# Kernel tuning notes

Measured on AMD Instinct MI355X. Metric: run time of the kernel, lower is better.

## Reference

```python
import jax, jax.numpy as jnp
import numpy as np

N_NODES = 100000


def _gcn_conv(x, row, col, W, b, n):
    # PyG GCNConv: h = W x; out_i = sum_{j->i} norm_ij * h_j + b, with self-loops
    # and symmetric normalization norm_ij = deg_i^-1/2 * deg_j^-1/2.
    h = x @ W  # [N, out]
    loop = jnp.arange(n, dtype=row.dtype)
    r = jnp.concatenate([row, loop])
    c = jnp.concatenate([col, loop])
    deg = jax.ops.segment_sum(jnp.ones_like(c, dtype=h.dtype), c, num_segments=n)
    dinv = jnp.where(deg > 0, jax.lax.rsqrt(deg), 0.0)
    norm = dinv[r] * dinv[c]  # [E+N]
    msg = h[r] * norm[:, None]  # gather + per-edge scale
    out = jax.ops.segment_sum(msg, c, num_segments=n)  # scatter-add to dst
    return out + b


def setup_inputs() -> dict:
    key = jax.random.key(0)
    ks = jax.random.split(key, 8)
    N, E = N_NODES, 1600000
    d_in, comm_dim, hid, out = 120, 8, 128, 64
    x = jax.random.normal(ks[0], (N, d_in), dtype=jnp.float32)
    edge_index = jax.random.randint(ks[1], (2, E), 0, N, dtype=jnp.int64)
    comm_ids = jax.random.randint(ks[2], (N,), 0, 64, dtype=jnp.int64)
    comm_emb = jax.random.normal(ks[3], (64, comm_dim), dtype=jnp.float32)
    s1 = 1.0 / np.sqrt(d_in + comm_dim)
    s2 = 1.0 / np.sqrt(hid)
    W1 = jax.random.normal(ks[4], (d_in + comm_dim, hid), dtype=jnp.float32) * s1
    b1 = jnp.zeros((hid,), dtype=jnp.float32)
    W2 = jax.random.normal(ks[5], (hid, out), dtype=jnp.float32) * s2
    b2 = jnp.zeros((out,), dtype=jnp.float32)
    return {"x": x, "edge_index": edge_index, "comm_ids": comm_ids,
            "comm_emb": comm_emb, "W1": W1, "b1": b1, "W2": W2, "b2": b2}


def reference(x, edge_index, comm_ids, comm_emb, W1, b1, W2, b2):
    n = x.shape[0]
    row, col = edge_index[0], edge_index[1]
    c = comm_emb[comm_ids]                      # [N, comm_dim] embedding lookup
    h = jnp.concatenate([x, c], axis=-1)        # [N, in+comm_dim]
    h = jax.nn.relu(_gcn_conv(h, row, col, W1, b1, n))
    # dropout p=0.5 is inactive in eval mode (training=False)
    out = _gcn_conv(h, row, col, W2, b2, n)     # [N, out_channels]
    return out
```

## Files before the change

kernel.cpp:

```cpp
#include <hip/hip_runtime.h>

typedef __attribute__((ext_vector_type(8))) short bf16x8;
typedef __attribute__((ext_vector_type(4))) float f32x4;

#define CAPB 5632
#define NBMAX 512

static __device__ __forceinline__ unsigned short f2bf(float f) {
    unsigned u = __float_as_uint(f);
    unsigned r = (u + 0x7fff + ((u >> 16) & 1)) >> 16;
    return (unsigned short)r;
}
static __device__ __forceinline__ float bfu_lo(unsigned v) { return __uint_as_float(v << 16); }
static __device__ __forceinline__ float bfu_hi(unsigned v) { return __uint_as_float(v & 0xffff0000u); }
static __device__ __forceinline__ unsigned packbf(float a, float b) {
    return (unsigned)f2bf(a) | ((unsigned)f2bf(b) << 16);
}

static __device__ __forceinline__ bf16x8 cvt8(float4 u0, float4 u1) {
    bf16x8 r;
    r[0] = (short)f2bf(u0.x); r[1] = (short)f2bf(u0.y);
    r[2] = (short)f2bf(u0.z); r[3] = (short)f2bf(u0.w);
    r[4] = (short)f2bf(u1.x); r[5] = (short)f2bf(u1.y);
    r[6] = (short)f2bf(u1.z); r[7] = (short)f2bf(u1.w);
    return r;
}

__global__ void k_zero_int(int* __restrict__ p, int n) {
    int i = blockIdx.x * blockDim.x + threadIdx.x;
    if (i < n) p[i] = 0;
}

__global__ __launch_bounds__(256) void k_passA(const int* __restrict__ row,
                                               const int* __restrict__ col,
                                               int* __restrict__ gcnt,
                                               unsigned* __restrict__ packed,
                                               int E, int NB) {
    __shared__ int lcnt[NBMAX];
    __shared__ int lbase[NBMAX];
    __shared__ int lcur[NBMAX];
    __shared__ int gbaseS[NBMAX];
    __shared__ unsigned stage[4096];
    __shared__ unsigned short stageb[4096];
    __shared__ int s[256];

    int tid = threadIdx.x;
    int t0 = blockIdx.x * 4096;
    int total = min(4096, E - t0);

    for (int b = tid; b < NBMAX; b += 256) { lcnt[b] = 0; lcur[b] = 0; }
    __syncthreads();

    int er[16], ec[16];
#pragma unroll
    for (int j = 0; j < 16; ++j) {
        int e = t0 + j * 256 + tid;
        if (e < E) {
            er[j] = row[e];
            ec[j] = col[e];
            atomicAdd(&lcnt[ec[j] >> 8], 1);
        }
    }
    __syncthreads();

    int c0 = lcnt[2 * tid], c1 = lcnt[2 * tid + 1];
    int p = c0 + c1;
    s[tid] = p;
    __syncthreads();
    for (int off = 1; off < 256; off <<= 1) {
        int t = (tid >= off) ? s[tid - off] : 0;
        __syncthreads();
        s[tid] += t;
        __syncthreads();
    }
    int ebase = s[tid] - p;
    lbase[2 * tid] = ebase;
    lbase[2 * tid + 1] = ebase + c0;
    __syncthreads();

    for (int b = tid; b < NB; b += 256) {
        int lc = lcnt[b];
        if (lc > 0) gbaseS[b] = atomicAdd(&gcnt[b], lc);
    }
    __syncthreads();

#pragma unroll
    for (int j = 0; j < 16; ++j) {
        int e = t0 + j * 256 + tid;
        if (e < E) {
            int b = ec[j] >> 8;
            int pos = lbase[b] + atomicAdd(&lcur[b], 1);
            stage[pos] = ((unsigned)er[j] << 8) | ((unsigned)ec[j] & 255u);
            stageb[pos] = (unsigned short)b;
        }
    }
    __syncthreads();

    for (int j = tid; j < total; j += 256) {
        int b = stageb[j];
        packed[(size_t)b * CAPB + gbaseS[b] + (j - lbase[b])] = stage[j];
    }
}

__global__ void k_bscan(const int* __restrict__ gcnt, int* __restrict__ gbase,
                        int* __restrict__ indptr, int n, int E, int NB) {
    __shared__ int s[512];
    int tid = threadIdx.x;
    int v = (tid < NB) ? gcnt[tid] : 0;
    s[tid] = v;
    __syncthreads();
    for (int off = 1; off < 512; off <<= 1) {
        int t = (tid >= off) ? s[tid - off] : 0;
        __syncthreads();
        s[tid] += t;
        __syncthreads();
    }
    if (tid < NB) gbase[tid] = s[tid] - v;
    if (tid == 0) indptr[n] = E;
}

__global__ __launch_bounds__(256) void k_passB(const unsigned* __restrict__ packed,
                                               const int* __restrict__ gcnt,
                                               const int* __restrict__ gbase,
                                               int* __restrict__ indptr,
                                               float* __restrict__ dinv,
                                               int* __restrict__ srcidx, int n) {
    __shared__ int ncnt[256];
    __shared__ int nbase[256];
    __shared__ int srow[CAPB];

    int b = blockIdx.x;
    int tid = threadIdx.x;
    int nodeBase = b << 8;
    int cntE = min(gcnt[b], CAPB);
    int base = gbase[b];
    size_t pb = (size_t)b * CAPB;

    ncnt[tid] = 0;
    __syncthreads();

    for (int j = tid; j < cntE; j += 256) {
        unsigned e = packed[pb + j];
        atomicAdd(&ncnt[e & 255u], 1);
    }
    __syncthreads();

    int v = ncnt[tid];
    nbase[tid] = v;
    __syncthreads();
    for (int off = 1; off < 256; off <<= 1) {
        int t = (tid >= off) ? nbase[tid - off] : 0;
        __syncthreads();
        nbase[tid] += t;
        __syncthreads();
    }
    int excl = nbase[tid] - v;
    __syncthreads();
    nbase[tid] = excl;

    int node = nodeBase + tid;
    if (node < n) {
        indptr[node] = base + excl;
        dinv[node] = rsqrtf((float)(v + 1));
    }
    ncnt[tid] = 0;
    __syncthreads();

    for (int j = tid; j < cntE; j += 256) {
        unsigned e = packed[pb + j];
        int c = (int)(e & 255u);
        int r = (int)(e >> 8);
        int p = nbase[c] + atomicAdd(&ncnt[c], 1);
        srow[p] = r;
    }
    __syncthreads();

    for (int j = tid; j < cntE; j += 256) srcidx[base + j] = srow[j];
}

__global__ void k_wprep(const float* __restrict__ W1, const float* __restrict__ W2,
                        const float* __restrict__ b1,
                        unsigned short* __restrict__ Wt1, unsigned short* __restrict__ Wt2p,
                        float* __restrict__ b1p) {
    int idx = blockIdx.x * blockDim.x + threadIdx.x;
    if (idx < 128 * 128) {
        int colc = idx >> 7, k = idx & 127;
        Wt1[colc * 128 + k] = f2bf(W1[k * 128 + colc]);
    } else if (idx < 128 * 128 + 64 * 128) {
        int j = idx - 128 * 128;
        int colc = j >> 7, p = j & 127;
        int korig = (p & 7) * 16 + (p >> 3);
        Wt2p[colc * 128 + p] = f2bf(W2[korig * 64 + colc]);
    } else if (idx < 128 * 128 + 64 * 128 + 128) {
        int p = idx - (128 * 128 + 64 * 128);
        b1p[p] = b1[(p & 7) * 16 + (p >> 3)];
    }
}

__global__ __launch_bounds__(256) void k_gemm1(const float* __restrict__ x,
                                               const int* __restrict__ cid,
                                               const float* __restrict__ cemb,
                                               const unsigned short* __restrict__ Wt,
                                               const float* __restrict__ dinv,
                                               unsigned char* __restrict__ D1q,
                                               float* __restrict__ scales, int n) {
    int tid = threadIdx.x;
    int wid = tid >> 6, lane = tid & 63;
    int rbase = blockIdx.x * 64 + wid * 16;
    int lr = lane & 15, kq = lane >> 4;

    int arow = rbase + lr;
    if (arow > n - 1) arow = n - 1;
    const float* xp = x + (size_t)arow * 120 + kq * 8;

    bf16x8 a0 = cvt8(*(const float4*)(xp),      *(const float4*)(xp + 4));
    bf16x8 a1 = cvt8(*(const float4*)(xp + 32), *(const float4*)(xp + 36));
    bf16x8 a2 = cvt8(*(const float4*)(xp + 64), *(const float4*)(xp + 68));
    bf16x8 a3;
    if (kq < 3) {
        a3 = cvt8(*(const float4*)(xp + 96), *(const float4*)(xp + 100));
    } else {
        const float* cp = cemb + (size_t)cid[arow] * 8;
        a3 = cvt8(*(const float4*)(cp), *(const float4*)(cp + 4));
    }

    f32x4 acc[8];
#pragma unroll
    for (int cf = 0; cf < 8; ++cf) acc[cf] = (f32x4){0.f, 0.f, 0.f, 0.f};

#pragma unroll
    for (int cf = 0; cf < 8; ++cf) {
        const unsigned short* bp = Wt + (size_t)(cf * 16 + lr) * 128 + kq * 8;
        bf16x8 b0 = *(const bf16x8*)(bp);
        bf16x8 b1 = *(const bf16x8*)(bp + 32);
        bf16x8 b2 = *(const bf16x8*)(bp + 64);
        bf16x8 b3 = *(const bf16x8*)(bp + 96);
        acc[cf] = __builtin_amdgcn_mfma_f32_16x16x32_bf16(a0, b0, acc[cf], 0, 0, 0);
        acc[cf] = __builtin_amdgcn_mfma_f32_16x16x32_bf16(a1, b1, acc[cf], 0, 0, 0);
        acc[cf] = __builtin_amdgcn_mfma_f32_16x16x32_bf16(a2, b2, acc[cf], 0, 0, 0);
        acc[cf] = __builtin_amdgcn_mfma_f32_16x16x32_bf16(a3, b3, acc[cf], 0, 0, 0);
    }

#pragma unroll
    for (int r = 0; r < 4; ++r) {
        int grow = rbase + kq * 4 + r;
        float dv = (grow < n) ? dinv[grow] : 0.f;
        float m = 0.f;
#pragma unroll
        for (int cf = 0; cf < 8; ++cf) m = fmaxf(m, fabsf(acc[cf][r] * dv));
        m = fmaxf(m, __shfl_xor(m, 1));
        m = fmaxf(m, __shfl_xor(m, 2));
        m = fmaxf(m, __shfl_xor(m, 4));
        m = fmaxf(m, __shfl_xor(m, 8));
        float sinv = (m > 1e-20f) ? 127.f / m : 0.f;
        if (grow < n) {
            if (lr == 0) scales[grow] = m * (1.f / 127.f);
            unsigned lo = 0, hi = 0;
#pragma unroll
            for (int cf = 0; cf < 4; ++cf) {
                int q8 = (int)rintf(acc[cf][r] * dv * sinv);
                lo |= ((unsigned)(q8 & 255)) << (8 * cf);
            }
#pragma unroll
            for (int cf = 4; cf < 8; ++cf) {
                int q8 = (int)rintf(acc[cf][r] * dv * sinv);
                hi |= ((unsigned)(q8 & 255)) << (8 * (cf - 4));
            }
            *(uint2*)&D1q[(size_t)grow * 128 + lr * 8] = make_uint2(lo, hi);
        }
    }
}

template <int NOUT>
__global__ __launch_bounds__(256) void k_gemm_bf16(const unsigned short* __restrict__ A,
                                                   const unsigned short* __restrict__ Wt,
                                                   const float* __restrict__ dinv,
                                                   unsigned short* __restrict__ D, int n) {
    constexpr int NCF = NOUT / 16;
    int tid = threadIdx.x;
    int wid = tid >> 6, lane = tid & 63;
    int rbase = blockIdx.x * 64 + wid * 16;
    int lr = lane & 15, kq = lane >> 4;

    int arow = rbase + lr;
    if (arow > n - 1) arow = n - 1;
    const unsigned short* ap = A + (size_t)arow * 128 + kq * 8;
    bf16x8 a0 = *(const bf16x8*)(ap);
    bf16x8 a1 = *(const bf16x8*)(ap + 32);
    bf16x8 a2 = *(const bf16x8*)(ap + 64);
    bf16x8 a3 = *(const bf16x8*)(ap + 96);

    f32x4 acc[NCF];
#pragma unroll
    for (int cf = 0; cf < NCF; ++cf) acc[cf] = (f32x4){0.f, 0.f, 0.f, 0.f};

#pragma unroll
    for (int cf = 0; cf < NCF; ++cf) {
        const unsigned short* bp = Wt + (size_t)(cf * 16 + lr) * 128 + kq * 8;
        bf16x8 b0 = *(const bf16x8*)(bp);
        bf16x8 b1 = *(const bf16x8*)(bp + 32);
        bf16x8 b2 = *(const bf16x8*)(bp + 64);
        bf16x8 b3 = *(const bf16x8*)(bp + 96);
        acc[cf] = __builtin_amdgcn_mfma_f32_16x16x32_bf16(a0, b0, acc[cf], 0, 0, 0);
        acc[cf] = __builtin_amdgcn_mfma_f32_16x16x32_bf16(a1, b1, acc[cf], 0, 0, 0);
        acc[cf] = __builtin_amdgcn_mfma_f32_16x16x32_bf16(a2, b2, acc[cf], 0, 0, 0);
        acc[cf] = __builtin_amdgcn_mfma_f32_16x16x32_bf16(a3, b3, acc[cf], 0, 0, 0);
    }

    float dv[4];
#pragma unroll
    for (int r = 0; r < 4; ++r) {
        int grow = rbase + kq * 4 + r;
        dv[r] = (grow < n) ? dinv[grow] : 0.f;
    }
#pragma unroll
    for (int cf = 0; cf < NCF; ++cf) {
#pragma unroll
        for (int r = 0; r < 4; ++r) {
            int grow = rbase + kq * 4 + r;
            if (grow < n) D[(size_t)grow * NOUT + cf * 16 + lr] = f2bf(acc[cf][r] * dv[r]);
        }
    }
}

__global__ __launch_bounds__(64) void k_agg1(const uint2* __restrict__ rows,
                                             const float* __restrict__ scales,
                                             const int* __restrict__ indptr,
                                             const int* __restrict__ srcidx,
                                             const float* __restrict__ dinv,
                                             const float* __restrict__ b1p,
                                             uint4* __restrict__ Out, int n) {
    int lane = threadIdx.x;
    int g = lane >> 4, gl = lane & 15;
    int i = blockIdx.x * 4 + g;
    if (i > n - 1) i = n - 1;

    float di = dinv[i];
    float4 bA = *(const float4*)&b1p[gl * 8];
    float4 bB = *(const float4*)&b1p[gl * 8 + 4];

    uint2 sq = rows[(size_t)i * 16 + gl];
    float ss = scales[i];
    float a[8];
#pragma unroll
    for (int j = 0; j < 4; ++j) {
        a[j]     = ss * (float)(signed char)((sq.x >> (8 * j)) & 255u);
        a[j + 4] = ss * (float)(signed char)((sq.y >> (8 * j)) & 255u);
    }

    int e0 = indptr[i];
    int d = indptr[i + 1] - e0;
    int m = max(d, __shfl_xor(d, 16));
    m = max(m, __shfl_xor(m, 32));

#pragma unroll 4
    for (int t = 0; t < m; ++t) {
        bool act = t < d;
        int s = act ? srcidx[e0 + t] : i;
        float sc = act ? scales[s] : 0.f;
        uint2 q = rows[(size_t)s * 16 + gl];
#pragma unroll
        for (int j = 0; j < 4; ++j) {
            a[j]     += sc * (float)(signed char)((q.x >> (8 * j)) & 255u);
            a[j + 4] += sc * (float)(signed char)((q.y >> (8 * j)) & 255u);
        }
    }

    uint4 o;
    o.x = packbf(fmaxf(di * a[0] + bA.x, 0.f), fmaxf(di * a[1] + bA.y, 0.f));
    o.y = packbf(fmaxf(di * a[2] + bA.z, 0.f), fmaxf(di * a[3] + bA.w, 0.f));
    o.z = packbf(fmaxf(di * a[4] + bB.x, 0.f), fmaxf(di * a[5] + bB.y, 0.f));
    o.w = packbf(fmaxf(di * a[6] + bB.z, 0.f), fmaxf(di * a[7] + bB.w, 0.f));
    Out[(size_t)i * 16 + gl] = o;
}

__global__ __launch_bounds__(64) void k_agg2(const uint2* __restrict__ Hs,
                                             const int* __restrict__ indptr,
                                             const int* __restrict__ srcidx,
                                             const float* __restrict__ dinv,
                                             const float* __restrict__ bias,
                                             float4* __restrict__ Out, int n) {
    int lane = threadIdx.x;
    int g = lane >> 4, gl = lane & 15;
    int i = blockIdx.x * 4 + g;
    if (i > n - 1) i = n - 1;

    float di = dinv[i];
    float4 b = *(const float4*)&bias[gl * 4];

    uint2 sv = Hs[(size_t)i * 16 + gl];
    float a0 = bfu_lo(sv.x), a1 = bfu_hi(sv.x);
    float a2 = bfu_lo(sv.y), a3 = bfu_hi(sv.y);

    int e0 = indptr[i];
    int d = indptr[i + 1] - e0;
    int m = max(d, __shfl_xor(d, 16));
    m = max(m, __shfl_xor(m, 32));

#pragma unroll 4
    for (int t = 0; t < m; ++t) {
        bool act = t < d;
        int s = act ? srcidx[e0 + t] : i;
        float msk = act ? 1.f : 0.f;
        uint2 w = Hs[(size_t)s * 16 + gl];
        a0 += msk * bfu_lo(w.x);
        a1 += msk * bfu_hi(w.x);
        a2 += msk * bfu_lo(w.y);
        a3 += msk * bfu_hi(w.y);
    }
    Out[(size_t)i * 16 + gl] = make_float4(di * a0 + b.x, di * a1 + b.y,
                                           di * a2 + b.z, di * a3 + b.w);
}


extern "C" void kernel_launch(void* const* d_in, const int* in_sizes, int n_in,
                              void* d_out, int out_size, void* d_ws, size_t ws_size,
                              hipStream_t stream) {
    const float* x    = (const float*)d_in[0];
    const int*   eidx = (const int*)d_in[1];
    const int*   cid  = (const int*)d_in[2];
    const float* cemb = (const float*)d_in[3];
    const float* W1   = (const float*)d_in[4];
    const float* b1   = (const float*)d_in[5];
    const float* W2   = (const float*)d_in[6];
    const float* b2   = (const float*)d_in[7];
    float* out = (float*)d_out;

    int n = in_sizes[2];
    int E = in_sizes[1] / 2;
    const int* row = eidx;
    const int* col = eidx + E;
    int NB = (n + 255) / 256;

    char* ws = (char*)d_ws;
    auto alloc = [&](size_t bytes) {
        char* p = ws;
        ws += (bytes + 255) & ~(size_t)255;
        return p;
    };
    float*          dinv   = (float*)alloc((size_t)n * 4);
    int*            gcnt   = (int*)alloc((size_t)NB * 4);
    int*            gbase  = (int*)alloc((size_t)NB * 4);
    int*            indptr = (int*)alloc((size_t)(n + 1) * 4);
    int*            srcidx = (int*)alloc((size_t)E * 4);
    unsigned*       packed = (unsigned*)alloc((size_t)NB * CAPB * 4);
    unsigned short* Wt1    = (unsigned short*)alloc(128 * 128 * 2);
    unsigned short* Wt2p   = (unsigned short*)alloc(64 * 128 * 2);
    float*          b1p    = (float*)alloc(128 * 4);
    unsigned char*  D1q    = (unsigned char*)alloc((size_t)n * 128);
    float*          scales = (float*)alloc((size_t)n * 4);
    unsigned short* H1p    = (unsigned short*)alloc((size_t)n * 128 * 2);
    unsigned short* D2     = (unsigned short*)alloc((size_t)n * 64 * 2);

    k_zero_int<<<(NB + 255) / 256, 256, 0, stream>>>(gcnt, NB);
    k_passA<<<(E + 4095) / 4096, 256, 0, stream>>>(row, col, gcnt, packed, E, NB);
    k_bscan<<<1, 512, 0, stream>>>(gcnt, gbase, indptr, n, E, NB);
    k_passB<<<NB, 256, 0, stream>>>(packed, gcnt, gbase, indptr, dinv, srcidx, n);

    k_wprep<<<(128 * 128 + 64 * 128 + 128 + 255) / 256, 256, 0, stream>>>(W1, W2, b1,
                                                                          Wt1, Wt2p, b1p);

    int gb = (n + 63) / 64;
    int ga = (n + 3) / 4;
    k_gemm1<<<gb, 256, 0, stream>>>(x, cid, cemb, Wt1, dinv, D1q, scales, n);
    k_agg1<<<ga, 64, 0, stream>>>((const uint2*)D1q, scales, indptr, srcidx, dinv, b1p,
                                  (uint4*)H1p, n);
    k_gemm_bf16<64><<<gb, 256, 0, stream>>>(H1p, Wt2p, dinv, D2, n);
    k_agg2<<<ga, 64, 0, stream>>>((const uint2*)D2, indptr, srcidx, dinv, b2,
                                  (float4*)out, n);
}
```

Baseline: 195.2 us.

## Use power-of-two int8 shifts with integer accumulation and zero sentinel rows

Replaces per-row float scales for the int8 layer-1 features with a per-row power-of-two shift exponent stored in one byte. Aggregation then accumulates in integers by shifting instead of converting and multiplying floats. Padding lanes read a zeroed sentinel row at index n, so the mask multiply goes away, and both aggregation kernels move from 64-thread to 256-thread blocks. This cuts per-edge ALU work and scale traffic, at the cost of coarser quantization scale (up to 2x range loss) and possible integer overflow risk at high degree.

Result: no change. 197.2 us (+1.0%).

```diff
diff --git a/kernel.cpp b/kernel.cpp
--- a/kernel.cpp
+++ b/kernel.cpp
@@ -181,19 +181,29 @@
 __global__ void k_wprep(const float* __restrict__ W1, const float* __restrict__ W2,
                         const float* __restrict__ b1,
                         unsigned short* __restrict__ Wt1, unsigned short* __restrict__ Wt2p,
-                        float* __restrict__ b1p) {
+                        float* __restrict__ b1p,
+                        unsigned* __restrict__ D1qz,
+                        unsigned* __restrict__ D2z,
+                        unsigned char* __restrict__ shifts, int n) {
     int idx = blockIdx.x * blockDim.x + threadIdx.x;
-    if (idx < 128 * 128) {
+    const int B0 = 128 * 128, B1 = B0 + 64 * 128, B2 = B1 + 128, B3 = B2 + 32, B4 = B3 + 32;
+    if (idx < B0) {
         int colc = idx >> 7, k = idx & 127;
         Wt1[colc * 128 + k] = f2bf(W1[k * 128 + colc]);
-    } else if (idx < 128 * 128 + 64 * 128) {
-        int j = idx - 128 * 128;
+    } else if (idx < B1) {
+        int j = idx - B0;
         int colc = j >> 7, p = j & 127;
         int korig = (p & 7) * 16 + (p >> 3);
         Wt2p[colc * 128 + p] = f2bf(W2[korig * 64 + colc]);
-    } else if (idx < 128 * 128 + 64 * 128 + 128) {
-        int p = idx - (128 * 128 + 64 * 128);
+    } else if (idx < B2) {
+        int p = idx - B1;
         b1p[p] = b1[(p & 7) * 16 + (p >> 3)];
+    } else if (idx < B3) {
+        D1qz[idx - B2] = 0;
+    } else if (idx < B4) {
+        D2z[idx - B3] = 0;
+    } else if (idx == B4) {
+        shifts[n] = 0;
     }
 }
 
@@ -203,7 +213,7 @@
                                                const unsigned short* __restrict__ Wt,
                                                const float* __restrict__ dinv,
                                                unsigned char* __restrict__ D1q,
-                                               float* __restrict__ scales, int n) {
+                                               unsigned char* __restrict__ shifts, int n) {
     int tid = threadIdx.x;
     int wid = tid >> 6, lane = tid & 63;
     int rbase = blockIdx.x * 64 + wid * 16;
@@ -252,18 +262,24 @@
         m = fmaxf(m, __shfl_xor(m, 2));
         m = fmaxf(m, __shfl_xor(m, 4));
         m = fmaxf(m, __shfl_xor(m, 8));
-        float sinv = (m > 1e-20f) ? 127.f / m : 0.f;
+        int mb = (int)((__float_as_uint(m) >> 23) & 255u);
+        int er = mb - 127 + 1 - 7;
+        int sh = min(max(er + 16, 0), 15);
+        int ee = sh - 16;
+        float sinv = __uint_as_float((unsigned)(127 - ee) << 23);
         if (grow < n) {
-            if (lr == 0) scales[grow] = m * (1.f / 127.f);
+            if (lr == 0) shifts[grow] = (unsigned char)sh;
             unsigned lo = 0, hi = 0;
 #pragma unroll
             for (int cf = 0; cf < 4; ++cf) {
                 int q8 = (int)rintf(acc[cf][r] * dv * sinv);
+                q8 = min(max(q8, -127), 127);
                 lo |= ((unsigned)(q8 & 255)) << (8 * cf);
             }
 #pragma unroll
             for (int cf = 4; cf < 8; ++cf) {
                 int q8 = (int)rintf(acc[cf][r] * dv * sinv);
+                q8 = min(max(q8, -127), 127);
                 hi |= ((unsigned)(q8 & 255)) << (8 * (cf - 4));
             }
             *(uint2*)&D1q[(size_t)grow * 128 + lr * 8] = make_uint2(lo, hi);
@@ -323,16 +339,17 @@
     }
 }
 
-__global__ __launch_bounds__(64) void k_agg1(const uint2* __restrict__ rows,
-                                             const float* __restrict__ scales,
-                                             const int* __restrict__ indptr,
-                                             const int* __restrict__ srcidx,
-                                             const float* __restrict__ dinv,
-                                             const float* __restrict__ b1p,
-                                             uint4* __restrict__ Out, int n) {
-    int lane = threadIdx.x;
+__global__ __launch_bounds__(256) void k_agg1(const uint2* __restrict__ rows,
+                                              const unsigned char* __restrict__ shifts,
+                                              const int* __restrict__ indptr,
+                                              const int* __restrict__ srcidx,
+                                              const float* __restrict__ dinv,
+                                              const float* __restrict__ b1p,
+                                              uint4* __restrict__ Out, int n) {
+    int tid = threadIdx.x;
+    int lane = tid & 63;
     int g = lane >> 4, gl = lane & 15;
-    int i = blockIdx.x * 4 + g;
+    int i = blockIdx.x * 16 + (tid >> 6) * 4 + g;
     if (i > n - 1) i = n - 1;
 
     float di = dinv[i];
@@ -340,12 +357,12 @@
     float4 bB = *(const float4*)&b1p[gl * 8 + 4];
 
     uint2 sq = rows[(size_t)i * 16 + gl];
-    float ss = scales[i];
-    float a[8];
+    int ssh = shifts[i];
+    int a[8];
 #pragma unroll
     for (int j = 0; j < 4; ++j) {
-        a[j]     = ss * (float)(signed char)((sq.x >> (8 * j)) & 255u);
-        a[j + 4] = ss * (float)(signed char)((sq.y >> (8 * j)) & 255u);
+        a[j]     = ((int)(signed char)((sq.x >> (8 * j)) & 255u)) << ssh;
+        a[j + 4] = ((int)(signed char)((sq.y >> (8 * j)) & 255u)) << ssh;
     }
 
     int e0 = indptr[i];
@@ -356,33 +373,35 @@
 #pragma unroll 4
     for (int t = 0; t < m; ++t) {
         bool act = t < d;
-        int s = act ? srcidx[e0 + t] : i;
-        float sc = act ? scales[s] : 0.f;
+        int s = act ? srcidx[e0 + t] : n;
+        int sh = shifts[s];
         uint2 q = rows[(size_t)s * 16 + gl];
 #pragma unroll
         for (int j = 0; j < 4; ++j) {
-            a[j]     += sc * (float)(signed char)((q.x >> (8 * j)) & 255u);
-            a[j + 4] += sc * (float)(signed char)((q.y >> (8 * j)) & 255u);
+            a[j]     += ((int)(signed char)((q.x >> (8 * j)) & 255u)) << sh;
+            a[j + 4] += ((int)(signed char)((q.y >> (8 * j)) & 255u)) << sh;
         }
     }
 
+    float sc = di * 0x1p-16f;
     uint4 o;
-    o.x = packbf(fmaxf(di * a[0] + bA.x, 0.f), fmaxf(di * a[1] + bA.y, 0.f));
-    o.y = packbf(fmaxf(di * a[2] + bA.z, 0.f), fmaxf(di * a[3] + bA.w, 0.f));
-    o.z = packbf(fmaxf(di * a[4] + bB.x, 0.f), fmaxf(di * a[5] + bB.y, 0.f));
-    o.w = packbf(fmaxf(di * a[6] + bB.z, 0.f), fmaxf(di * a[7] + bB.w, 0.f));
+    o.x = packbf(fmaxf((float)a[0] * sc + bA.x, 0.f), fmaxf((float)a[1] * sc + bA.y, 0.f));
+    o.y = packbf(fmaxf((float)a[2] * sc + bA.z, 0.f), fmaxf((float)a[3] * sc + bA.w, 0.f));
+    o.z = packbf(fmaxf((float)a[4] * sc + bB.x, 0.f), fmaxf((float)a[5] * sc + bB.y, 0.f));
+    o.w = packbf(fmaxf((float)a[6] * sc + bB.z, 0.f), fmaxf((float)a[7] * sc + bB.w, 0.f));
     Out[(size_t)i * 16 + gl] = o;
 }
 
-__global__ __launch_bounds__(64) void k_agg2(const uint2* __restrict__ Hs,
-                                             const int* __restrict__ indptr,
-                                             const int* __restrict__ srcidx,
-                                             const float* __restrict__ dinv,
-                                             const float* __restrict__ bias,
-                                             float4* __restrict__ Out, int n) {
-    int lane = threadIdx.x;
+__global__ __launch_bounds__(256) void k_agg2(const uint2* __restrict__ Hs,
+                                              const int* __restrict__ indptr,
+                                              const int* __restrict__ srcidx,
+                                              const float* __restrict__ dinv,
+                                              const float* __restrict__ bias,
+                                              float4* __restrict__ Out, int n) {
+    int tid = threadIdx.x;
+    int lane = tid & 63;
     int g = lane >> 4, gl = lane & 15;
-    int i = blockIdx.x * 4 + g;
+    int i = blockIdx.x * 16 + (tid >> 6) * 4 + g;
     if (i > n - 1) i = n - 1;
 
     float di = dinv[i];
@@ -400,13 +419,12 @@
 #pragma unroll 4
     for (int t = 0; t < m; ++t) {
         bool act = t < d;
-        int s = act ? srcidx[e0 + t] : i;
-        float msk = act ? 1.f : 0.f;
+        int s = act ? srcidx[e0 + t] : n;
         uint2 w = Hs[(size_t)s * 16 + gl];
-        a0 += msk * bfu_lo(w.x);
-        a1 += msk * bfu_hi(w.x);
-        a2 += msk * bfu_lo(w.y);
-        a3 += msk * bfu_hi(w.y);
+        a0 += bfu_lo(w.x);
+        a1 += bfu_hi(w.x);
+        a2 += bfu_lo(w.y);
+        a3 += bfu_hi(w.y);
     }
     Out[(size_t)i * 16 + gl] = make_float4(di * a0 + b.x, di * a1 + b.y,
                                            di * a2 + b.z, di * a3 + b.w);
@@ -447,25 +465,29 @@
     unsigned short* Wt1    = (unsigned short*)alloc(128 * 128 * 2);
     unsigned short* Wt2p   = (unsigned short*)alloc(64 * 128 * 2);
     float*          b1p    = (float*)alloc(128 * 4);
-    unsigned char*  D1q    = (unsigned char*)alloc((size_t)n * 128);
-    float*          scales = (float*)alloc((size_t)n * 4);
+    unsigned char*  D1q    = (unsigned char*)alloc((size_t)(n + 1) * 128);
+    unsigned char*  shifts = (unsigned char*)alloc((size_t)(n + 1));
     unsigned short* H1p    = (unsigned short*)alloc((size_t)n * 128 * 2);
-    unsigned short* D2     = (unsigned short*)alloc((size_t)n * 64 * 2);
+    unsigned short* D2     = (unsigned short*)alloc((size_t)(n + 1) * 64 * 2);
 
     k_zero_int<<<(NB + 255) / 256, 256, 0, stream>>>(gcnt, NB);
     k_passA<<<(E + 4095) / 4096, 256, 0, stream>>>(row, col, gcnt, packed, E, NB);
     k_bscan<<<1, 512, 0, stream>>>(gcnt, gbase, indptr, n, E, NB);
     k_passB<<<NB, 256, 0, stream>>>(packed, gcnt, gbase, indptr, dinv, srcidx, n);
 
-    k_wprep<<<(128 * 128 + 64 * 128 + 128 + 255) / 256, 256, 0, stream>>>(W1, W2, b1,
-                                                                          Wt1, Wt2p, b1p);
+    int wpn = 128 * 128 + 64 * 128 + 128 + 32 + 32 + 1;
+    k_wprep<<<(wpn + 255) / 256, 256, 0, stream>>>(
+        W1, W2, b1, Wt1, Wt2p, b1p,
+        (unsigned*)(D1q + (size_t)n * 128),
+        (unsigned*)(D2 + (size_t)n * 64),
+        shifts, n);
 
     int gb = (n + 63) / 64;
-    int ga = (n + 3) / 4;
-    k_gemm1<<<gb, 256, 0, stream>>>(x, cid, cemb, Wt1, dinv, D1q, scales, n);
-    k_agg1<<<ga, 64, 0, stream>>>((const uint2*)D1q, scales, indptr, srcidx, dinv, b1p,
-                                  (uint4*)H1p, n);
+    int ga = (n + 15) / 16;
+    k_gemm1<<<gb, 256, 0, stream>>>(x, cid, cemb, Wt1, dinv, D1q, shifts, n);
+    k_agg1<<<ga, 256, 0, stream>>>((const uint2*)D1q, shifts, indptr, srcidx, dinv, b1p,
+                                   (uint4*)H1p, n);
     k_gemm_bf16<64><<<gb, 256, 0, stream>>>(H1p, Wt2p, dinv, D2, n);
-    k_agg2<<<ga, 64, 0, stream>>>((const uint2*)D2, indptr, srcidx, dinv, b2,
-                                  (float4*)out, n);
-}
+    k_agg2<<<ga, 256, 0, stream>>>((const uint2*)D2, indptr, srcidx, dinv, b2,
+                                   (float4*)out, n);
+}
```
